# Kernel tuning notes

Measured on AMD Instinct MI355X. Metric: run time of the kernel, lower is better.

Reference implementation:

```python
import jax, jax.numpy as jnp
import numpy as np

NUM_INSTANCES = 64  # instance ids in [0, 64); id 0 is background and excluded


def _variance_smooth_loss(variances, ins_labels, num_segments):
    # variances: [N, D] float, ins_labels: [N] int
    N, D = variances.shape
    ones = jnp.ones((N,), dtype=variances.dtype)
    counts = jax.ops.segment_sum(ones, ins_labels, num_segments=num_segments)          # [S]
    sums = jax.ops.segment_sum(variances, ins_labels, num_segments=num_segments)       # [S, D]
    safe_counts = jnp.maximum(counts, 1.0)
    means = sums / safe_counts[:, None]                                                # per-instance mean [S, D]
    diff = variances - means[ins_labels]                                               # gather means back [N, D]
    sq = jnp.sum(diff * diff, axis=1)                                                  # [N]
    # per-instance MSE = sum of squared diffs / (K_i * D), matching nn.MSELoss (mean reduction)
    per_ins = jax.ops.segment_sum(sq, ins_labels, num_segments=num_segments) / (safe_counts * D)
    valid = (counts > 0) & (jnp.arange(num_segments) != 0)                             # skip id 0 & absent ids
    return jnp.sum(jnp.where(valid, per_ins, jnp.zeros_like(per_ins)))


def setup_inputs() -> dict:
    key = jax.random.key(0)
    k1, k2 = jax.random.split(key)
    N, D = 4_000_000, 8
    variances = jax.random.normal(k1, (N, D), dtype=jnp.float32)
    ins_labels = jax.random.randint(k2, (N,), 0, NUM_INSTANCES, dtype=jnp.int32)
    return {"variances": variances, "ins_labels": ins_labels}


def reference(variances, ins_labels):
    return _variance_smooth_loss(variances, ins_labels, NUM_INSTANCES)
```

## Files before the change

kernel.cpp:

```cpp
#include <hip/hip_runtime.h>

#define NUM_INST 64
#define SLOT 12
#define NSLOT 65
#define BLOCK 256
#define NWAVES 4
#define GRID 1792

typedef float f32x4 __attribute__((ext_vector_type(4)));
typedef float f32x2 __attribute__((ext_vector_type(2)));

__device__ __forceinline__ void pk_add(f32x2& acc, f32x2 v) {
    asm("v_pk_add_f32 %0, %0, %1" : "+v"(acc) : "v"(v));
}
__device__ __forceinline__ void pk_fma_sq(f32x2& acc, f32x2 v) {
    asm("v_pk_fma_f32 %0, %1, %1, %0" : "+v"(acc) : "v"(v));
}

__global__ __launch_bounds__(BLOCK) void vsl_main(const f32x4* __restrict__ rows,
                                                  const int* __restrict__ labels,
                                                  float* __restrict__ gacc, int n) {
    __shared__ float lds[NWAVES][NSLOT * SLOT];
    const int tid = threadIdx.x;
    const int w = tid >> 6;
    const int lane = tid & 63;
    float* const wbase = &lds[w][0];

    if (lane < 9) wbase[64 * SLOT + lane] = 0.0f;

    f32x2 acc01 = {0, 0}, acc23 = {0, 0}, acc45 = {0, 0}, acc67 = {0, 0};
    float ssq = 0, cntf = 0;

    float* const pub = wbase + lane * SLOT;
    const int stride = GRID * BLOCK;

    int i = blockIdx.x * BLOCK + tid;
    bool valid = (i < n);
    unsigned long long bv = __ballot(valid);
    int lbl = 0;
    f32x4 a = {0, 0, 0, 0}, b = {0, 0, 0, 0};
    if (valid) { lbl = labels[i]; a = rows[2 * i]; b = rows[2 * i + 1]; }

    while (bv) {
        const int inext = i + stride;
        const bool vnext = (inext < n);
        const unsigned long long bvn = __ballot(vnext);
        int lbln = 0;
        f32x4 an = {0, 0, 0, 0}, bn = {0, 0, 0, 0};
        if (vnext) { lbln = labels[inext]; an = rows[2 * inext]; bn = rows[2 * inext + 1]; }

        f32x2 sq2 = {0, 0};
        pk_fma_sq(sq2, __builtin_shufflevector(a, a, 0, 1));
        pk_fma_sq(sq2, __builtin_shufflevector(a, a, 2, 3));
        pk_fma_sq(sq2, __builtin_shufflevector(b, b, 0, 1));
        pk_fma_sq(sq2, __builtin_shufflevector(b, b, 2, 3));
        const float sq = sq2.x + sq2.y;

        *(f32x4*)pub = a;
        *(f32x4*)(pub + 4) = b;
        pub[8] = sq;

        unsigned long long m = bv;
#pragma unroll
        for (int bpos = 0; bpos < 6; ++bpos) {
            const unsigned long long bb = __ballot((lbl >> bpos) & 1);
            m &= ((lane >> bpos) & 1) ? bb : ~bb;
        }
        cntf += (float)__popcll(m);

        unsigned mlo = (unsigned)m;
        unsigned mhi = (unsigned)(m >> 32);

        asm volatile("s_waitcnt lgkmcnt(0)" ::: "memory");

        while (mlo | mhi) {
            unsigned slo, shi;
            asm("v_ffbl_b32 %0, %1" : "=v"(slo) : "v"(mlo));
            asm("v_ffbl_b32 %0, %1" : "=v"(shi) : "v"(mhi));
            const unsigned s = min(slo, min(shi, 32u) + 32u);
            const bool uselo = (mlo != 0);
            const unsigned nlo = mlo & (mlo - 1);
            const unsigned nhi = mhi & (mhi - 1);
            mlo = nlo;
            mhi = uselo ? mhi : nhi;
            const float* sp = wbase + s * SLOT;
            const f32x4 p = *(const f32x4*)sp;
            const f32x4 q = *(const f32x4*)(sp + 4);
            const float r = sp[8];
            pk_add(acc01, __builtin_shufflevector(p, p, 0, 1));
            pk_add(acc23, __builtin_shufflevector(p, p, 2, 3));
            pk_add(acc45, __builtin_shufflevector(q, q, 0, 1));
            pk_add(acc67, __builtin_shufflevector(q, q, 2, 3));
            ssq += r;
        }

        i = inext; bv = bvn; lbl = lbln; a = an; b = bn;
    }

    float* fb = wbase + lane * SLOT;
    fb[0] = acc01.x; fb[1] = acc01.y; fb[2] = acc23.x; fb[3] = acc23.y;
    fb[4] = acc45.x; fb[5] = acc45.y; fb[6] = acc67.x; fb[7] = acc67.y;
    fb[8] = ssq; fb[9] = cntf;
    __syncthreads();

    for (int j = tid; j < NUM_INST * 10; j += BLOCK) {
        const int L = j / 10;
        const int st = j - L * 10;
        float v = 0;
#pragma unroll
        for (int ww = 0; ww < NWAVES; ++ww) v += lds[ww][L * SLOT + st];
        atomicAdd(&gacc[j], v);
    }
}

__global__ __launch_bounds__(64) void vsl_final(const float* __restrict__ gacc,
                                                float* __restrict__ out) {
    const int s = threadIdx.x;
    float val = 0.0f;
    const float* base = &gacc[s * 10];
    const float cnt = base[9];
    if (s != 0 && cnt > 0.0f) {
        const float ss = base[8];
        float m2 = 0.0f;
#pragma unroll
        for (int d = 0; d < 8; ++d) {
            const float sd = base[d];
            m2 += sd * sd;
        }
        val = (ss - m2 / cnt) / (cnt * 8.0f);
    }
#pragma unroll
    for (int off = 32; off > 0; off >>= 1) val += __shfl_down(val, off, 64);
    if (s == 0) out[0] = val;
}

extern "C" void kernel_launch(void* const* d_in, const int* in_sizes, int n_in,
                              void* d_out, int out_size, void* d_ws, size_t ws_size,
                              hipStream_t stream) {
    const float* variances = (const float*)d_in[0];
    const int* labels = (const int*)d_in[1];
    const int n = in_sizes[1];
    float* gacc = (float*)d_ws;

    hipMemsetAsync(d_ws, 0, NUM_INST * 10 * sizeof(float), stream);
    vsl_main<<<GRID, BLOCK, 0, stream>>>((const f32x4*)variances, labels, gacc, n);
    vsl_final<<<1, 64, 0, stream>>>(gacc, (float*)d_out);
}
```

Measured before the change: 223.8 us.

## Batch three rows per lane per phase and drain four matches per iteration

```diff
diff --git a/kernel.cpp b/kernel.cpp
--- a/kernel.cpp
+++ b/kernel.cpp
@@ -2,10 +2,12 @@
 
 #define NUM_INST 64
 #define SLOT 12
-#define NSLOT 65
+#define RCH 3
+#define ZSLOT (RCH * 64)
+#define NSLOT (ZSLOT + 1)
 #define BLOCK 256
 #define NWAVES 4
-#define GRID 1792
+#define GRID 1024
 
 typedef float f32x4 __attribute__((ext_vector_type(4)));
 typedef float f32x2 __attribute__((ext_vector_type(2)));
@@ -17,90 +19,131 @@
     asm("v_pk_fma_f32 %0, %1, %1, %0" : "+v"(acc) : "v"(v));
 }
 
-__global__ __launch_bounds__(BLOCK) void vsl_main(const f32x4* __restrict__ rows,
-                                                  const int* __restrict__ labels,
-                                                  float* __restrict__ gacc, int n) {
+__device__ __forceinline__ int take3(unsigned long long& m0, unsigned long long& m1,
+                                     unsigned long long& m2) {
+    const bool u0 = (m0 != 0), u1 = (m1 != 0);
+    const unsigned long long sel = u0 ? m0 : (u1 ? m1 : m2);
+    const int base = u0 ? 0 : (u1 ? 64 : 128);
+    const int s = sel ? (base + (int)__builtin_ctzll(sel)) : ZSLOT;
+    const unsigned long long cl = sel & (sel - 1);
+    m0 = u0 ? cl : m0;
+    m1 = (!u0 && u1) ? cl : m1;
+    m2 = (!u0 && !u1) ? cl : m2;
+    return s;
+}
+
+__global__ __launch_bounds__(BLOCK, 4) void vsl_main(const f32x4* __restrict__ rows,
+                                                     const int* __restrict__ labels,
+                                                     float* __restrict__ gacc, int n) {
     __shared__ float lds[NWAVES][NSLOT * SLOT];
     const int tid = threadIdx.x;
     const int w = tid >> 6;
     const int lane = tid & 63;
     float* const wbase = &lds[w][0];
 
-    if (lane < 9) wbase[64 * SLOT + lane] = 0.0f;
+    if (lane < 8) wbase[ZSLOT * SLOT + lane] = 0.0f;
 
     f32x2 acc01 = {0, 0}, acc23 = {0, 0}, acc45 = {0, 0}, acc67 = {0, 0};
-    float ssq = 0, cntf = 0;
+    f32x2 ssq2 = {0, 0};
+    float cntf = 0;
 
-    float* const pub = wbase + lane * SLOT;
-    const int stride = GRID * BLOCK;
+    f32x4* const pub0 = (f32x4*)(wbase + lane * SLOT);
+    f32x4* const pub1 = (f32x4*)(wbase + (64 + lane) * SLOT);
+    f32x4* const pub2 = (f32x4*)(wbase + (128 + lane) * SLOT);
 
-    int i = blockIdx.x * BLOCK + tid;
-    bool valid = (i < n);
-    unsigned long long bv = __ballot(valid);
-    int lbl = 0;
-    f32x4 a = {0, 0, 0, 0}, b = {0, 0, 0, 0};
-    if (valid) { lbl = labels[i]; a = rows[2 * i]; b = rows[2 * i + 1]; }
+    const int S = GRID * BLOCK;
+    const int phaseStride = RCH * S;
+    const int nph = (n + phaseStride - 1) / phaseStride;
 
-    while (bv) {
-        const int inext = i + stride;
-        const bool vnext = (inext < n);
-        const unsigned long long bvn = __ballot(vnext);
-        int lbln = 0;
-        f32x4 an = {0, 0, 0, 0}, bn = {0, 0, 0, 0};
-        if (vnext) { lbln = labels[inext]; an = rows[2 * inext]; bn = rows[2 * inext + 1]; }
+    int i0 = blockIdx.x * BLOCK + tid;
+    for (int ph = 0; ph < nph; ++ph, i0 += phaseStride) {
+        const int i1 = i0 + S;
+        const int i2 = i1 + S;
+        const bool v0 = (i0 < n), v1 = (i1 < n), v2 = (i2 < n);
 
-        f32x2 sq2 = {0, 0};
-        pk_fma_sq(sq2, __builtin_shufflevector(a, a, 0, 1));
-        pk_fma_sq(sq2, __builtin_shufflevector(a, a, 2, 3));
-        pk_fma_sq(sq2, __builtin_shufflevector(b, b, 0, 1));
-        pk_fma_sq(sq2, __builtin_shufflevector(b, b, 2, 3));
-        const float sq = sq2.x + sq2.y;
+        int l0 = 0, l1 = 0, l2 = 0;
+        f32x4 a0 = {0, 0, 0, 0}, b0 = {0, 0, 0, 0};
+        f32x4 a1 = {0, 0, 0, 0}, b1 = {0, 0, 0, 0};
+        f32x4 a2 = {0, 0, 0, 0}, b2 = {0, 0, 0, 0};
+        if (v0) { l0 = labels[i0]; a0 = rows[2 * i0]; b0 = rows[2 * i0 + 1]; }
+        if (v1) { l1 = labels[i1]; a1 = rows[2 * i1]; b1 = rows[2 * i1 + 1]; }
+        if (v2) { l2 = labels[i2]; a2 = rows[2 * i2]; b2 = rows[2 * i2 + 1]; }
 
-        *(f32x4*)pub = a;
-        *(f32x4*)(pub + 4) = b;
-        pub[8] = sq;
+        pub0[0] = a0; pub0[1] = b0;
+        pub1[0] = a1; pub1[1] = b1;
+        pub2[0] = a2; pub2[1] = b2;
 
-        unsigned long long m = bv;
+        unsigned long long m0 = __ballot(v0), m1 = __ballot(v1), m2 = __ballot(v2);
 #pragma unroll
         for (int bpos = 0; bpos < 6; ++bpos) {
-            const unsigned long long bb = __ballot((lbl >> bpos) & 1);
-            m &= ((lane >> bpos) & 1) ? bb : ~bb;
+            const unsigned long long t0 = __ballot((l0 >> bpos) & 1);
+            const unsigned long long t1 = __ballot((l1 >> bpos) & 1);
+            const unsigned long long t2 = __ballot((l2 >> bpos) & 1);
+            const bool mybit = (lane >> bpos) & 1;
+            m0 &= mybit ? t0 : ~t0;
+            m1 &= mybit ? t1 : ~t1;
+            m2 &= mybit ? t2 : ~t2;
         }
-        cntf += (float)__popcll(m);
-
-        unsigned mlo = (unsigned)m;
-        unsigned mhi = (unsigned)(m >> 32);
+        cntf += (float)(__popcll(m0) + __popcll(m1) + __popcll(m2));
 
         asm volatile("s_waitcnt lgkmcnt(0)" ::: "memory");
 
-        while (mlo | mhi) {
-            unsigned slo, shi;
-            asm("v_ffbl_b32 %0, %1" : "=v"(slo) : "v"(mlo));
-            asm("v_ffbl_b32 %0, %1" : "=v"(shi) : "v"(mhi));
-            const unsigned s = min(slo, min(shi, 32u) + 32u);
-            const bool uselo = (mlo != 0);
-            const unsigned nlo = mlo & (mlo - 1);
-            const unsigned nhi = mhi & (mhi - 1);
-            mlo = nlo;
-            mhi = uselo ? mhi : nhi;
-            const float* sp = wbase + s * SLOT;
-            const f32x4 p = *(const f32x4*)sp;
-            const f32x4 q = *(const f32x4*)(sp + 4);
-            const float r = sp[8];
-            pk_add(acc01, __builtin_shufflevector(p, p, 0, 1));
-            pk_add(acc23, __builtin_shufflevector(p, p, 2, 3));
-            pk_add(acc45, __builtin_shufflevector(q, q, 0, 1));
-            pk_add(acc67, __builtin_shufflevector(q, q, 2, 3));
-            ssq += r;
+        while (m0 | m1 | m2) {
+            const int s0 = take3(m0, m1, m2);
+            const int s1 = take3(m0, m1, m2);
+            const int s2 = take3(m0, m1, m2);
+            const int s3 = take3(m0, m1, m2);
+            const f32x4* q0 = (const f32x4*)(wbase + s0 * SLOT);
+            const f32x4* q1 = (const f32x4*)(wbase + s1 * SLOT);
+            const f32x4* q2 = (const f32x4*)(wbase + s2 * SLOT);
+            const f32x4* q3 = (const f32x4*)(wbase + s3 * SLOT);
+            const f32x4 pa0 = q0[0], pb0 = q0[1];
+            const f32x4 pa1 = q1[0], pb1 = q1[1];
+            const f32x4 pa2 = q2[0], pb2 = q2[1];
+            const f32x4 pa3 = q3[0], pb3 = q3[1];
+
+            pk_add(acc01, __builtin_shufflevector(pa0, pa0, 0, 1));
+            pk_add(acc23, __builtin_shufflevector(pa0, pa0, 2, 3));
+            pk_add(acc45, __builtin_shufflevector(pb0, pb0, 0, 1));
+            pk_add(acc67, __builtin_shufflevector(pb0, pb0, 2, 3));
+            pk_fma_sq(ssq2, __builtin_shufflevector(pa0, pa0, 0, 1));
+            pk_fma_sq(ssq2, __builtin_shufflevector(pa0, pa0, 2, 3));
+            pk_fma_sq(ssq2, __builtin_shufflevector(pb0, pb0, 0, 1));
+            pk_fma_sq(ssq2, __builtin_shufflevector(pb0, pb0, 2, 3));
+
+            pk_add(acc01, __builtin_shufflevector(pa1, pa1, 0, 1));
+            pk_add(acc23, __builtin_shufflevector(pa1, pa1, 2, 3));
+            pk_add(acc45, __builtin_shufflevector(pb1, pb1, 0, 1));
+            pk_add(acc67, __builtin_shufflevector(pb1, pb1, 2, 3));
+            pk_fma_sq(ssq2, __builtin_shufflevector(pa1, pa1, 0, 1));
+            pk_fma_sq(ssq2, __builtin_shufflevector(pa1, pa1, 2, 3));
+            pk_fma_sq(ssq2, __builtin_shufflevector(pb1, pb1, 0, 1));
+            pk_fma_sq(ssq2, __builtin_shufflevector(pb1, pb1, 2, 3));
+
+            pk_add(acc01, __builtin_shufflevector(pa2, pa2, 0, 1));
+            pk_add(acc23, __builtin_shufflevector(pa2, pa2, 2, 3));
+            pk_add(acc45, __builtin_shufflevector(pb2, pb2, 0, 1));
+            pk_add(acc67, __builtin_shufflevector(pb2, pb2, 2, 3));
+            pk_fma_sq(ssq2, __builtin_shufflevector(pa2, pa2, 0, 1));
+            pk_fma_sq(ssq2, __builtin_shufflevector(pa2, pa2, 2, 3));
+            pk_fma_sq(ssq2, __builtin_shufflevector(pb2, pb2, 0, 1));
+            pk_fma_sq(ssq2, __builtin_shufflevector(pb2, pb2, 2, 3));
+
+            pk_add(acc01, __builtin_shufflevector(pa3, pa3, 0, 1));
+            pk_add(acc23, __builtin_shufflevector(pa3, pa3, 2, 3));
+            pk_add(acc45, __builtin_shufflevector(pb3, pb3, 0, 1));
+            pk_add(acc67, __builtin_shufflevector(pb3, pb3, 2, 3));
+            pk_fma_sq(ssq2, __builtin_shufflevector(pa3, pa3, 0, 1));
+            pk_fma_sq(ssq2, __builtin_shufflevector(pa3, pa3, 2, 3));
+            pk_fma_sq(ssq2, __builtin_shufflevector(pb3, pb3, 0, 1));
+            pk_fma_sq(ssq2, __builtin_shufflevector(pb3, pb3, 2, 3));
         }
-
-        i = inext; bv = bvn; lbl = lbln; a = an; b = bn;
     }
 
     float* fb = wbase + lane * SLOT;
     fb[0] = acc01.x; fb[1] = acc01.y; fb[2] = acc23.x; fb[3] = acc23.y;
     fb[4] = acc45.x; fb[5] = acc45.y; fb[6] = acc67.x; fb[7] = acc67.y;
-    fb[8] = ssq; fb[9] = cntf;
+    fb[8] = ssq2.x + ssq2.y; fb[9] = cntf;
     __syncthreads();
 
     for (int j = tid; j < NUM_INST * 10; j += BLOCK) {
```

New measurement: 206.3 us. 1.09x faster.
